# Kernel tuning notes

Hardware: AMD Instinct MI355X
Metric: run time of the kernel (lower is better)

The kernel has to match this reference:

```python
import jax, jax.numpy as jnp
import numpy as np
import math

B, S, D, H = 2, 2048, 1024, 16
HD = D // H
WINDOW_LEFT = 256   # window_size=(256,-1): only left constraint active
NEG = -1e9


def rotate_half(x):
    x1, x2 = jnp.split(x, 2, axis=-1)
    return jnp.concatenate([-x2, x1], axis=-1)


def setup_inputs() -> dict:
    key = jax.random.key(0)
    ks = jax.random.split(key, 10)
    x = jax.random.normal(ks[0], (B, S, D), dtype=jnp.float32)
    mask = jnp.ones((B, S), dtype=bool)
    cos = jax.random.uniform(ks[1], (B, S, HD), dtype=jnp.float32)
    sin = jax.random.uniform(ks[2], (B, S, HD), dtype=jnp.float32)
    sc = 1.0 / math.sqrt(D)
    Wq = jax.random.normal(ks[3], (D, D), dtype=jnp.float32) * sc
    bq = jax.random.normal(ks[4], (D,), dtype=jnp.float32) * 0.02
    Wk = jax.random.normal(ks[5], (D, D), dtype=jnp.float32) * sc
    Wv = jax.random.normal(ks[6], (D, D), dtype=jnp.float32) * sc
    bv = jax.random.normal(ks[7], (D,), dtype=jnp.float32) * 0.02
    Wo = jax.random.normal(ks[8], (D, D), dtype=jnp.float32) * sc
    bo = jax.random.normal(ks[9], (D,), dtype=jnp.float32) * 0.02
    return {"x": x, "mask": mask, "cos": cos, "sin": sin,
            "Wq": Wq, "bq": bq, "Wk": Wk, "Wv": Wv, "bv": bv,
            "Wo": Wo, "bo": bo}


def reference(x, mask, cos, sin, Wq, bq, Wk, Wv, bv, Wo, bo):
    batch, seq_len, embed_dim = x.shape
    scale = 1.0 / math.sqrt(HD)

    q = x @ Wq + bq          # [b,s,d], bias on q
    k = x @ Wk               # no bias on k
    v = x @ Wv + bv          # bias on v

    def split_heads(t):
        return jnp.swapaxes(t.reshape(batch, seq_len, H, HD), 1, 2)  # [b,h,s,hd]

    q, k, v = split_heads(q), split_heads(k), split_heads(v)

    c = cos[:, None, :, :]   # [b,1,s,hd]
    s_ = sin[:, None, :, :]
    q = q * c + rotate_half(q) * s_
    k = k * c + rotate_half(k) * s_

    scores = jnp.einsum('bhqd,bhkd->bhqk', q, k) * scale
    # padding mask over keys
    scores = jnp.where(mask[:, None, None, :], scores, NEG)
    # causal + sliding-window (left=256) masks combined
    pos = jnp.arange(seq_len)
    rel = pos[None, :] - pos[:, None]          # k - q
    keep = (rel <= 0) & (rel >= -WINDOW_LEFT)  # causal AND window-left
    scores = jnp.where(keep, scores, NEG)

    weights = jax.nn.softmax(scores, axis=-1)
    context = jnp.einsum('bhqk,bhkd->bhqd', weights, v)
    context = jnp.swapaxes(context, 1, 2).reshape(batch, seq_len, embed_dim)
    out = context @ Wo + bo
    out = out * mask[..., None]
    return out
```

## Files before the change

kernel.cpp:

```cpp
#include <hip/hip_runtime.h>
#include <cstdint>
#include <cstddef>

typedef __bf16 bf16;
typedef bf16 bf16x4 __attribute__((ext_vector_type(4)));
typedef bf16 bf16x8 __attribute__((ext_vector_type(8)));
typedef float f32x4 __attribute__((ext_vector_type(4)));

#define S_LEN 2048
#define DIM   1024
#define NHEAD 16
#define HDIM  64

__device__ __forceinline__ f32x4 mfma16(bf16x8 a, bf16x8 b, f32x4 c) {
    return __builtin_amdgcn_mfma_f32_16x16x32_bf16(a, b, c, 0, 0, 0);
}

__device__ __forceinline__ float exp2fast(float x) {
    return __builtin_amdgcn_exp2f(x);
}

__device__ __forceinline__ void gload_lds16(const bf16* g, bf16* l) {
    __builtin_amdgcn_global_load_lds(
        (const __attribute__((address_space(1))) unsigned*)g,
        (__attribute__((address_space(3))) unsigned*)l, 16, 0, 0);
}

__global__ __launch_bounds__(256) void cvt_x_kernel(const float* __restrict__ x,
                                                    bf16* __restrict__ xb) {
    int i = blockIdx.x * 256 + threadIdx.x;
    float4 v = ((const float4*)x)[i];
    bf16x4 o = { (bf16)v.x, (bf16)v.y, (bf16)v.z, (bf16)v.w };
    ((bf16x4*)xb)[i] = o;
}

__global__ __launch_bounds__(256) void wt_kernel(const float* __restrict__ Wq, const float* __restrict__ Wk,
                                                 const float* __restrict__ Wv, const float* __restrict__ Wo,
                                                 bf16* __restrict__ WqT, bf16* __restrict__ WkT,
                                                 bf16* __restrict__ WvT, bf16* __restrict__ WoT) {
    const float* W; bf16* WT;
    int z = blockIdx.z;
    if      (z == 0) { W = Wq; WT = WqT; }
    else if (z == 1) { W = Wk; WT = WkT; }
    else if (z == 2) { W = Wv; WT = WvT; }
    else             { W = Wo; WT = WoT; }
    __shared__ bf16 tile[64][72];
    int k0 = blockIdx.x * 64, n0 = blockIdx.y * 64;
    int t = threadIdx.x;
#pragma unroll
    for (int p = 0; p < 4; ++p) {
        int task = p * 256 + t;
        int ki = task >> 4, nj = (task & 15) * 4;
        float4 v = *(const float4*)(W + (size_t)(k0 + ki) * DIM + n0 + nj);
        tile[ki][nj + 0] = (bf16)v.x; tile[ki][nj + 1] = (bf16)v.y;
        tile[ki][nj + 2] = (bf16)v.z; tile[ki][nj + 3] = (bf16)v.w;
    }
    __syncthreads();
#pragma unroll
    for (int p = 0; p < 4; ++p) {
        int task = p * 256 + t;
        int ni = task >> 4, kj = (task & 15) * 4;
        bf16x4 o = { tile[kj + 0][ni], tile[kj + 1][ni], tile[kj + 2][ni], tile[kj + 3][ni] };
        *(bf16x4*)(WT + (size_t)(n0 + ni) * DIM + k0 + kj) = o;
    }
}

__device__ __forceinline__ void stage256(const bf16* __restrict__ A, const bf16* __restrict__ BT,
                                         int m0, int n0, int k0, int t, int w, bf16* dst) {
#pragma unroll
    for (int i = 0; i < 4; ++i) {
        int c = i * 512 + t;
        int row = c >> 3;
        int colb = ((c & 7) * 16) ^ ((row & 7) << 4);
        gload_lds16(A + (size_t)(m0 + row) * DIM + k0 + (colb >> 1), dst + i * 4096 + w * 512);
    }
#pragma unroll
    for (int i = 0; i < 4; ++i) {
        int c = i * 512 + t;
        int row = c >> 3;
        int colb = ((c & 7) * 16) ^ ((row & 7) << 4);
        gload_lds16(BT + (size_t)(n0 + row) * DIM + k0 + (colb >> 1), dst + 16384 + i * 4096 + w * 512);
    }
}

__global__ __launch_bounds__(512, 2) void gemm_qkv_kernel(const bf16* __restrict__ xb,
                                                          const bf16* __restrict__ WallT,
                                                          const float* __restrict__ bq, const float* __restrict__ bv,
                                                          const float* __restrict__ cosp, const float* __restrict__ sinp,
                                                          bf16* __restrict__ qT, bf16* __restrict__ kT,
                                                          bf16* __restrict__ vT) {
    __shared__ bf16 lds[2][32768];
    int t = threadIdx.x, lane = t & 63, w = t >> 6;
    int wr = w >> 2, wc = w & 3;
    int lc = lane & 15, lr = lane >> 4;
    int bid = blockIdx.x;
    int swz = (bid & 7) * 24 + (bid >> 3);
    int bx = swz / 12, by = swz % 12;
    int m0 = bx * 256, n0 = by * 256;

    f32x4 acc[8][4] = {};
    const int aswz = (lc & 7) << 4;

    stage256(xb, WallT, m0, n0, 0, t, w, lds[0]);
    asm volatile("s_waitcnt vmcnt(0)" ::: "memory");
    __builtin_amdgcn_s_barrier();
    __builtin_amdgcn_sched_barrier(0);

    const int NT = DIM / 64;
    for (int kt = 0; kt < NT; ++kt) {
        if (kt + 1 < NT) stage256(xb, WallT, m0, n0, (kt + 1) * 64, t, w, lds[(kt + 1) & 1]);
        const char* bufb = (const char*)lds[kt & 1];
        bf16x8 aF[4], bF[4];
#pragma unroll
        for (int ks = 0; ks < 2; ++ks) {
#pragma unroll
            for (int nf = 0; nf < 4; ++nf) {
                int row = wc * 64 + nf * 16 + lc;
                bF[nf] = *(const bf16x8*)(bufb + 32768 + ((row * 128 + ks * 64 + lr * 16) ^ aswz));
            }
#pragma unroll
            for (int half = 0; half < 2; ++half) {
#pragma unroll
                for (int m4 = 0; m4 < 4; ++m4) {
                    int row = wr * 128 + (half * 4 + m4) * 16 + lc;
                    aF[m4] = *(const bf16x8*)(bufb + ((row * 128 + ks * 64 + lr * 16) ^ aswz));
                }
                __builtin_amdgcn_s_setprio(1);
#pragma unroll
                for (int m4 = 0; m4 < 4; ++m4)
#pragma unroll
                    for (int nf = 0; nf < 4; ++nf)
                        acc[half * 4 + m4][nf] = mfma16(aF[m4], bF[nf], acc[half * 4 + m4][nf]);
                __builtin_amdgcn_s_setprio(0);
            }
        }
        if (kt + 1 < NT) {
            asm volatile("s_waitcnt vmcnt(0)" ::: "memory");
            __builtin_amdgcn_s_barrier();
            __builtin_amdgcn_sched_barrier(0);
        }
    }

    int z = by >> 2;
    int h = (by & 3) * 4 + wc;
    int row0 = m0 + wr * 128 + lr * 4;
    if (z < 2) {
        bf16* qkT = (z == 0) ? qT : kT;
#pragma unroll
        for (int nf = 0; nf < 2; ++nf) {
            int hd1 = nf * 16 + lc;
            float b1 = (z == 0) ? bq[h * HDIM + hd1] : 0.0f;
            float b2 = (z == 0) ? bq[h * HDIM + hd1 + 32] : 0.0f;
#pragma unroll
            for (int mf = 0; mf < 8; ++mf) {
#pragma unroll
                for (int r = 0; r < 4; ++r) {
                    int bs = row0 + mf * 16 + r;
                    size_t cb = (size_t)bs * HDIM + hd1;
                    float c1 = cosp[cb], s1 = sinp[cb];
                    float c2 = cosp[cb + 32], s2 = sinp[cb + 32];
                    float v1 = acc[mf][nf][r] + b1;
                    float v2 = acc[mf][nf + 2][r] + b2;
                    int b = bs >> 11, s = bs & (S_LEN - 1);
                    size_t o = ((size_t)(b * NHEAD + h) * S_LEN + s) * HDIM;
                    qkT[o + hd1]      = (bf16)(v1 * c1 - v2 * s1);
                    qkT[o + hd1 + 32] = (bf16)(v2 * c2 + v1 * s2);
                }
            }
        }
    } else {
#pragma unroll
        for (int nf = 0; nf < 4; ++nf) {
            int hd = nf * 16 + lc;
            float bvv = bv[h * HDIM + hd];
#pragma unroll
            for (int mf = 0; mf < 8; ++mf) {
                bf16x4 o;
#pragma unroll
                for (int r = 0; r < 4; ++r) o[r] = (bf16)(acc[mf][nf][r] + bvv);
                int bs = row0 + mf * 16;
                int b = bs >> 11, s = bs & (S_LEN - 1);
                *(bf16x4*)(vT + ((size_t)((b * NHEAD + h) * HDIM + hd)) * S_LEN + s) = o;
            }
        }
    }
}

__device__ __forceinline__ void stage_tile(const bf16* __restrict__ A, const bf16* __restrict__ BT,
                                           int m0, int n0, int k0,
                                           bf16* sA, bf16* sB, int w, int lane) {
#pragma unroll
    for (int p = 0; p < 2; ++p) {
        int c = p * 256 + w * 64 + lane;
        const bf16* ga = A + (size_t)(m0 + (c >> 2)) * DIM + k0 + (c & 3) * 8;
        gload_lds16(ga, sA + (p * 256 + w * 64) * 8);
        const bf16* gb = BT + (size_t)(n0 + (c >> 2)) * DIM + k0 + (c & 3) * 8;
        gload_lds16(gb, sB + (p * 256 + w * 64) * 8);
    }
}

__device__ __forceinline__ void gemm_main(const bf16* __restrict__ A, const bf16* __restrict__ BT,
                                          int m0, int n0, f32x4 acc[4][4]) {
    __shared__ bf16 sA[3][128 * 32];
    __shared__ bf16 sB[3][128 * 32];
    int t = threadIdx.x;
    int lane = t & 63, w = t >> 6;
    int wr = w >> 1, wc = w & 1;
    int lc = lane & 15, lr = lane >> 4;
    const int NSTEP = DIM / 32;

    stage_tile(A, BT, m0, n0, 0,  sA[0], sB[0], w, lane);
    stage_tile(A, BT, m0, n0, 32, sA[1], sB[1], w, lane);

    int rs = 0, ss = 2;
    for (int kt = 0; kt < NSTEP; ++kt) {
        if (kt < NSTEP - 1) asm volatile("s_waitcnt vmcnt(4)" ::: "memory");
        else                asm volatile("s_waitcnt vmcnt(0)" ::: "memory");
        __builtin_amdgcn_s_barrier();
        asm volatile("" ::: "memory");
        if (kt < NSTEP - 2)
            stage_tile(A, BT, m0, n0, (kt + 2) * 32, sA[ss], sB[ss], w, lane);

        const bf16* pa = sA[rs] + (wr * 64 + lc) * 32 + lr * 8;
        const bf16* pb = sB[rs] + (wc * 64 + lc) * 32 + lr * 8;
        bf16x8 af[4], bfr[4];
#pragma unroll
        for (int m = 0; m < 4; ++m) af[m] = *(const bf16x8*)(pa + m * 16 * 32);
#pragma unroll
        for (int n = 0; n < 4; ++n) bfr[n] = *(const bf16x8*)(pb + n * 16 * 32);
#pragma unroll
        for (int m = 0; m < 4; ++m)
#pragma unroll
            for (int n = 0; n < 4; ++n)
                acc[m][n] = mfma16(af[m], bfr[n], acc[m][n]);
        rs = (rs == 2) ? 0 : rs + 1;
        ss = (ss == 2) ? 0 : ss + 1;
    }
}

__global__ __launch_bounds__(256, 3) void gemm_out_kernel(const bf16* __restrict__ ctx, const bf16* __restrict__ WoT,
                                                          const float* __restrict__ bo, float* __restrict__ out) {
    int m0 = blockIdx.x * 128, n0 = blockIdx.y * 128;
    f32x4 acc[4][4] = {};
    gemm_main(ctx, WoT, m0, n0, acc);
    int t = threadIdx.x;
    int lane = t & 63, w = t >> 6;
    int wr = w >> 1, wc = w & 1;
    int lc = lane & 15, lr = lane >> 4;
    int row0 = m0 + wr * 64 + lr * 4;
    int col0 = n0 + wc * 64 + lc;
#pragma unroll
    for (int nf = 0; nf < 4; ++nf) {
        int col = col0 + nf * 16;
        float bvv = bo[col];
#pragma unroll
        for (int mf = 0; mf < 4; ++mf)
#pragma unroll
            for (int r = 0; r < 4; ++r)
                out[(size_t)(row0 + mf * 16 + r) * DIM + col] = acc[mf][nf][r] + bvv;
    }
}

__global__ __launch_bounds__(64) void attn_kernel(const bf16* __restrict__ qT, const bf16* __restrict__ kT,
                                                  const bf16* __restrict__ vT, bf16* __restrict__ ctx) {
    int q0 = blockIdx.x * 32;
    int bh = blockIdx.y;
    int b = bh >> 4, h = bh & 15;
    int lane = threadIdx.x;
    int lc = lane & 15, lr = lane >> 4;
    __shared__ bf16 sP[32 * 64];
    char* sPb = (char*)sP;
    const bf16* Qb = qT + (size_t)bh * S_LEN * HDIM;
    const bf16* Kb = kT + (size_t)bh * S_LEN * HDIM;
    const bf16* Vb = vT + (size_t)bh * HDIM * S_LEN;

    const float SCL = 0.125f * 1.44269504089f;
    const int swz = (lc & 7) << 4;

    bf16x8 qf[2][2];
#pragma unroll
    for (int mf = 0; mf < 2; ++mf)
#pragma unroll
        for (int kk = 0; kk < 2; ++kk)
            qf[mf][kk] = *(const bf16x8*)(Qb + (size_t)(q0 + mf * 16 + lc) * HDIM + kk * 32 + lr * 8);

    f32x4 accO[2][4] = {};
    float mrun[2] = { -30000.0f, -30000.0f };
    float lrun[2] = { 0.0f, 0.0f };

    int klo = (q0 >= 256) ? ((q0 - 256) >> 6) : 0;
    int khi = (q0 + 31) >> 6;

    bf16x8 kfc[8], kfn[8], vf[8];
#pragma unroll
    for (int nf = 0; nf < 4; ++nf)
#pragma unroll
        for (int kk = 0; kk < 2; ++kk)
            kfc[nf * 2 + kk] = *(const bf16x8*)(Kb + (size_t)(klo * 64 + nf * 16 + lc) * HDIM + kk * 32 + lr * 8);

    for (int kt = klo; kt <= khi; ++kt) {
        int kbase = kt * 64;
#pragma unroll
        for (int n4 = 0; n4 < 4; ++n4)
#pragma unroll
            for (int kk = 0; kk < 2; ++kk)
                vf[n4 * 2 + kk] = *(const bf16x8*)(Vb + (size_t)(n4 * 16 + lc) * S_LEN + kbase + kk * 32 + lr * 8);
        if (kt < khi) {
#pragma unroll
            for (int nf = 0; nf < 4; ++nf)
#pragma unroll
                for (int kk = 0; kk < 2; ++kk)
                    kfn[nf * 2 + kk] = *(const bf16x8*)(Kb + (size_t)(kbase + 64 + nf * 16 + lc) * HDIM + kk * 32 + lr * 8);
        }

        f32x4 sacc[2][4] = {};
        __builtin_amdgcn_s_setprio(1);
#pragma unroll
        for (int nf = 0; nf < 4; ++nf)
#pragma unroll
            for (int kk = 0; kk < 2; ++kk) {
                sacc[0][nf] = mfma16(kfc[nf * 2 + kk], qf[0][kk], sacc[0][nf]);
                sacc[1][nf] = mfma16(kfc[nf * 2 + kk], qf[1][kk], sacc[1][nf]);
            }
        __builtin_amdgcn_s_setprio(0);
#pragma unroll
        for (int mf = 0; mf < 2; ++mf) {
            int qi = q0 + mf * 16 + lc;
#pragma unroll
            for (int nf = 0; nf < 4; ++nf)
#pragma unroll
                for (int r = 0; r < 4; ++r) {
                    int ki = kbase + nf * 16 + lr * 4 + r;
                    bool keep = (ki <= qi) && (ki >= qi - 256);
                    sacc[mf][nf][r] = keep ? sacc[mf][nf][r] * SCL : -30000.0f;
                }
        }
#pragma unroll
        for (int mf = 0; mf < 2; ++mf) {
            float mx = sacc[mf][0][0];
#pragma unroll
            for (int nf = 0; nf < 4; ++nf)
#pragma unroll
                for (int r = 0; r < 4; ++r) mx = fmaxf(mx, sacc[mf][nf][r]);
            mx = fmaxf(mx, __shfl_xor(mx, 16));
            mx = fmaxf(mx, __shfl_xor(mx, 32));
            float mnew = fmaxf(mrun[mf], mx);
            float alpha = exp2fast(mrun[mf] - mnew);
            mrun[mf] = mnew;
            float rsum = 0.0f;
#pragma unroll
            for (int nf = 0; nf < 4; ++nf)
#pragma unroll
                for (int r = 0; r < 4; ++r) {
                    float e = exp2fast(sacc[mf][nf][r] - mnew);
                    sacc[mf][nf][r] = e;
                    rsum += e;
                }
            rsum += __shfl_xor(rsum, 16);
            rsum += __shfl_xor(rsum, 32);
            lrun[mf] = lrun[mf] * alpha + rsum;
            float aq[4];
#pragma unroll
            for (int r = 0; r < 4; ++r) aq[r] = __shfl(alpha, lr * 4 + r);
#pragma unroll
            for (int n4 = 0; n4 < 4; ++n4)
#pragma unroll
                for (int r = 0; r < 4; ++r) accO[mf][n4][r] *= aq[r];
        }
#pragma unroll
        for (int mf = 0; mf < 2; ++mf)
#pragma unroll
            for (int nf = 0; nf < 4; ++nf) {
                bf16x4 o = { (bf16)sacc[mf][nf][0], (bf16)sacc[mf][nf][1],
                             (bf16)sacc[mf][nf][2], (bf16)sacc[mf][nf][3] };
                int wb = ((mf * 16 + lc) * 64 + nf * 16 + lr * 4) * 2;
                *(bf16x4*)(sPb + (wb ^ swz)) = o;
            }
        asm volatile("s_waitcnt lgkmcnt(0)" ::: "memory");
        bf16x8 pf[2][2];
#pragma unroll
        for (int mf = 0; mf < 2; ++mf)
#pragma unroll
            for (int kk = 0; kk < 2; ++kk) {
                int rb = ((mf * 16 + lc) * 64 + kk * 32 + lr * 8) * 2;
                pf[mf][kk] = *(const bf16x8*)(sPb + (rb ^ swz));
            }
        __builtin_amdgcn_s_setprio(1);
#pragma unroll
        for (int n4 = 0; n4 < 4; ++n4)
#pragma unroll
            for (int kk = 0; kk < 2; ++kk) {
                accO[0][n4] = mfma16(pf[0][kk], vf[n4 * 2 + kk], accO[0][n4]);
                accO[1][n4] = mfma16(pf[1][kk], vf[n4 * 2 + kk], accO[1][n4]);
            }
        __builtin_amdgcn_s_setprio(0);
#pragma unroll
        for (int i = 0; i < 8; ++i) kfc[i] = kfn[i];
    }
#pragma unroll
    for (int mf = 0; mf < 2; ++mf) {
        float linv = 1.0f / lrun[mf];
        float lq[4];
#pragma unroll
        for (int r = 0; r < 4; ++r) lq[r] = __shfl(linv, lr * 4 + r);
#pragma unroll
        for (int n4 = 0; n4 < 4; ++n4)
#pragma unroll
            for (int r = 0; r < 4; ++r) {
                int s = q0 + mf * 16 + lr * 4 + r;
                int d = n4 * 16 + lc;
                ctx[((size_t)(b * S_LEN + s)) * DIM + h * HDIM + d] = (bf16)(accO[mf][n4][r] * lq[r]);
            }
    }
}

extern "C" void kernel_launch(void* const* d_in, const int* in_sizes, int n_in,
                              void* d_out, int out_size, void* d_ws, size_t ws_size,
                              hipStream_t stream) {
    const float* x    = (const float*)d_in[0];
    const float* cosp = (const float*)d_in[2];
    const float* sinp = (const float*)d_in[3];
    const float* Wq   = (const float*)d_in[4];
    const float* bq   = (const float*)d_in[5];
    const float* Wk   = (const float*)d_in[6];
    const float* Wv   = (const float*)d_in[7];
    const float* bv   = (const float*)d_in[8];
    const float* Wo   = (const float*)d_in[9];
    const float* bo   = (const float*)d_in[10];
    float* out = (float*)d_out;

    char* ws = (char*)d_ws;
    const size_t MB = 1ull << 20;
    bf16* xb  = (bf16*)(ws + 0 * MB);
    bf16* WqT = (bf16*)(ws + 8 * MB);
    bf16* WkT = (bf16*)(ws + 10 * MB);
    bf16* WvT = (bf16*)(ws + 12 * MB);
    bf16* WoT = (bf16*)(ws + 14 * MB);
    bf16* qT  = (bf16*)(ws + 16 * MB);
    bf16* kT  = (bf16*)(ws + 24 * MB);
    bf16* vT  = (bf16*)(ws + 32 * MB);
    bf16* ctx = (bf16*)(ws + 40 * MB);

    cvt_x_kernel<<<4096, 256, 0, stream>>>(x, xb);
    wt_kernel<<<dim3(16, 16, 4), 256, 0, stream>>>(Wq, Wk, Wv, Wo, WqT, WkT, WvT, WoT);
    gemm_qkv_kernel<<<192, 512, 0, stream>>>(xb, WqT, bq, bv, cosp, sinp, qT, kT, vT);
    attn_kernel<<<dim3(64, 32), 64, 0, stream>>>(qT, kT, vT, ctx);
    gemm_out_kernel<<<dim3(32, 8), 256, 0, stream>>>(ctx, WoT, bo, out);
}
```

Measured before the change: 103.9 us.

## Split QKV GEMM K-stages into half-units with finer-grained pipelined loads and XCD-aware attention mapping

Restructures the QKV GEMM main loop so each 64-wide K step is loaded as two 32-wide units. The second unit is issued after the first is consumed, with vmcnt-based partial waits instead of a full drain each step. It also changes the LDS swizzle to a 64-element row layout, removes the L2-oriented block swizzle in the QKV GEMM, and remaps attention blocks so heads are grouped per XCD. The weight pointer is renamed from WallT to Wall, which may imply a layout change on the host side not shown here. The extra barriers per step add sync overhead in exchange for better overlap of loads and MFMA work.

```diff
diff --git a/kernel.cpp b/kernel.cpp
--- a/kernel.cpp
+++ b/kernel.cpp
@@ -65,26 +65,8 @@
     }
 }
 
-__device__ __forceinline__ void stage256(const bf16* __restrict__ A, const bf16* __restrict__ BT,
-                                         int m0, int n0, int k0, int t, int w, bf16* dst) {
-#pragma unroll
-    for (int i = 0; i < 4; ++i) {
-        int c = i * 512 + t;
-        int row = c >> 3;
-        int colb = ((c & 7) * 16) ^ ((row & 7) << 4);
-        gload_lds16(A + (size_t)(m0 + row) * DIM + k0 + (colb >> 1), dst + i * 4096 + w * 512);
-    }
-#pragma unroll
-    for (int i = 0; i < 4; ++i) {
-        int c = i * 512 + t;
-        int row = c >> 3;
-        int colb = ((c & 7) * 16) ^ ((row & 7) << 4);
-        gload_lds16(BT + (size_t)(n0 + row) * DIM + k0 + (colb >> 1), dst + 16384 + i * 4096 + w * 512);
-    }
-}
-
 __global__ __launch_bounds__(512, 2) void gemm_qkv_kernel(const bf16* __restrict__ xb,
-                                                          const bf16* __restrict__ WallT,
+                                                          const bf16* __restrict__ Wall,
                                                           const float* __restrict__ bq, const float* __restrict__ bv,
                                                           const float* __restrict__ cosp, const float* __restrict__ sinp,
                                                           bf16* __restrict__ qT, bf16* __restrict__ kT,
@@ -94,52 +76,96 @@
     int wr = w >> 2, wc = w & 3;
     int lc = lane & 15, lr = lane >> 4;
     int bid = blockIdx.x;
-    int swz = (bid & 7) * 24 + (bid >> 3);
-    int bx = swz / 12, by = swz % 12;
+    int bx = bid / 12, by = bid % 12;
     int m0 = bx * 256, n0 = by * 256;
 
+    int i0 = t, i1 = 512 + t;
+    int r0 = i0 >> 2, r1 = i1 >> 2;
+    int ke0 = (((i0 & 3) ^ (r0 & 3)) << 3);
+    int ke1 = (((i1 & 3) ^ (r1 & 3)) << 3);
+    const bf16* srcA0 = xb   + (size_t)(m0 + r0) * DIM + ke0;
+    const bf16* srcA1 = xb   + (size_t)(m0 + r1) * DIM + ke1;
+    const bf16* srcB0 = Wall + (size_t)(n0 + r0) * DIM + ke0;
+    const bf16* srcB1 = Wall + (size_t)(n0 + r1) * DIM + ke1;
+
+#define STAGE_UNIT(kt_, u_) {                                              \
+        bf16* d = (bf16*)lds[(kt_) & 1] + (u_) * 8192 + w * 512;           \
+        int ko = (kt_) * 64 + (u_) * 32;                                   \
+        gload_lds16(srcA0 + ko, d);                                        \
+        gload_lds16(srcB0 + ko, d + 16384);                                \
+        gload_lds16(srcA1 + ko, d + 4096);                                 \
+        gload_lds16(srcB1 + ko, d + 4096 + 16384);                         \
+    }
+
     f32x4 acc[8][4] = {};
-    const int aswz = (lc & 7) << 4;
-
-    stage256(xb, WallT, m0, n0, 0, t, w, lds[0]);
-    asm volatile("s_waitcnt vmcnt(0)" ::: "memory");
-    __builtin_amdgcn_s_barrier();
-    __builtin_amdgcn_sched_barrier(0);
+    const int aoff = (lr * 16) ^ ((lc & 3) << 4);
+    const int arow = (wr * 128 + lc) * 64;
+    const int brow = 32768 + (wc * 64 + lc) * 64;
 
     const int NT = DIM / 64;
+    STAGE_UNIT(0, 0);
+    STAGE_UNIT(0, 1);
+
     for (int kt = 0; kt < NT; ++kt) {
-        if (kt + 1 < NT) stage256(xb, WallT, m0, n0, (kt + 1) * 64, t, w, lds[(kt + 1) & 1]);
-        const char* bufb = (const char*)lds[kt & 1];
+        asm volatile("s_waitcnt vmcnt(4)" ::: "memory");
+        __builtin_amdgcn_s_barrier();
+        asm volatile("" ::: "memory");
+        if (kt + 1 < NT) STAGE_UNIT(kt + 1, 0);
+        const char* base = (const char*)lds[kt & 1];
         bf16x8 aF[4], bF[4];
 #pragma unroll
-        for (int ks = 0; ks < 2; ++ks) {
-#pragma unroll
-            for (int nf = 0; nf < 4; ++nf) {
-                int row = wc * 64 + nf * 16 + lc;
-                bF[nf] = *(const bf16x8*)(bufb + 32768 + ((row * 128 + ks * 64 + lr * 16) ^ aswz));
-            }
-#pragma unroll
-            for (int half = 0; half < 2; ++half) {
-#pragma unroll
-                for (int m4 = 0; m4 < 4; ++m4) {
-                    int row = wr * 128 + (half * 4 + m4) * 16 + lc;
-                    aF[m4] = *(const bf16x8*)(bufb + ((row * 128 + ks * 64 + lr * 16) ^ aswz));
-                }
-                __builtin_amdgcn_s_setprio(1);
-#pragma unroll
-                for (int m4 = 0; m4 < 4; ++m4)
-#pragma unroll
-                    for (int nf = 0; nf < 4; ++nf)
-                        acc[half * 4 + m4][nf] = mfma16(aF[m4], bF[nf], acc[half * 4 + m4][nf]);
-                __builtin_amdgcn_s_setprio(0);
-            }
-        }
-        if (kt + 1 < NT) {
-            asm volatile("s_waitcnt vmcnt(0)" ::: "memory");
-            __builtin_amdgcn_s_barrier();
-            __builtin_amdgcn_sched_barrier(0);
-        }
-    }
+        for (int nf = 0; nf < 4; ++nf)
+            bF[nf] = *(const bf16x8*)(base + brow + nf * 1024 + aoff);
+#pragma unroll
+        for (int m4 = 0; m4 < 4; ++m4)
+            aF[m4] = *(const bf16x8*)(base + arow + m4 * 1024 + aoff);
+        __builtin_amdgcn_s_setprio(1);
+#pragma unroll
+        for (int m4 = 0; m4 < 4; ++m4)
+#pragma unroll
+            for (int nf = 0; nf < 4; ++nf)
+                acc[m4][nf] = mfma16(aF[m4], bF[nf], acc[m4][nf]);
+        __builtin_amdgcn_s_setprio(0);
+#pragma unroll
+        for (int m4 = 0; m4 < 4; ++m4)
+            aF[m4] = *(const bf16x8*)(base + arow + 4096 + m4 * 1024 + aoff);
+        __builtin_amdgcn_s_setprio(1);
+#pragma unroll
+        for (int m4 = 0; m4 < 4; ++m4)
+#pragma unroll
+            for (int nf = 0; nf < 4; ++nf)
+                acc[4 + m4][nf] = mfma16(aF[m4], bF[nf], acc[4 + m4][nf]);
+        __builtin_amdgcn_s_setprio(0);
+        if (kt + 1 < NT) asm volatile("s_waitcnt vmcnt(4)" ::: "memory");
+        else             asm volatile("s_waitcnt vmcnt(0)" ::: "memory");
+        __builtin_amdgcn_s_barrier();
+        asm volatile("" ::: "memory");
+        if (kt + 1 < NT) STAGE_UNIT(kt + 1, 1);
+#pragma unroll
+        for (int nf = 0; nf < 4; ++nf)
+            bF[nf] = *(const bf16x8*)(base + 16384 + brow + nf * 1024 + aoff);
+#pragma unroll
+        for (int m4 = 0; m4 < 4; ++m4)
+            aF[m4] = *(const bf16x8*)(base + 16384 + arow + m4 * 1024 + aoff);
+        __builtin_amdgcn_s_setprio(1);
+#pragma unroll
+        for (int m4 = 0; m4 < 4; ++m4)
+#pragma unroll
+            for (int nf = 0; nf < 4; ++nf)
+                acc[m4][nf] = mfma16(aF[m4], bF[nf], acc[m4][nf]);
+        __builtin_amdgcn_s_setprio(0);
+#pragma unroll
+        for (int m4 = 0; m4 < 4; ++m4)
+            aF[m4] = *(const bf16x8*)(base + 16384 + arow + 4096 + m4 * 1024 + aoff);
+        __builtin_amdgcn_s_setprio(1);
+#pragma unroll
+        for (int m4 = 0; m4 < 4; ++m4)
+#pragma unroll
+            for (int nf = 0; nf < 4; ++nf)
+                acc[4 + m4][nf] = mfma16(aF[m4], bF[nf], acc[4 + m4][nf]);
+        __builtin_amdgcn_s_setprio(0);
+    }
+#undef STAGE_UNIT
 
     int z = by >> 2;
     int h = (by & 3) * 4 + wc;
@@ -199,18 +225,20 @@
     }
 }
 
-__device__ __forceinline__ void gemm_main(const bf16* __restrict__ A, const bf16* __restrict__ BT,
-                                          int m0, int n0, f32x4 acc[4][4]) {
+__global__ __launch_bounds__(256, 3) void gemm_out_kernel(const bf16* __restrict__ ctx, const bf16* __restrict__ WoT,
+                                                          const float* __restrict__ bo, float* __restrict__ out) {
     __shared__ bf16 sA[3][128 * 32];
     __shared__ bf16 sB[3][128 * 32];
+    int m0 = blockIdx.x * 128, n0 = blockIdx.y * 128;
     int t = threadIdx.x;
     int lane = t & 63, w = t >> 6;
     int wr = w >> 1, wc = w & 1;
     int lc = lane & 15, lr = lane >> 4;
     const int NSTEP = DIM / 32;
 
-    stage_tile(A, BT, m0, n0, 0,  sA[0], sB[0], w, lane);
-    stage_tile(A, BT, m0, n0, 32, sA[1], sB[1], w, lane);
+    f32x4 acc[4][4] = {};
+    stage_tile(ctx, WoT, m0, n0, 0,  sA[0], sB[0], w, lane);
+    stage_tile(ctx, WoT, m0, n0, 32, sA[1], sB[1], w, lane);
 
     int rs = 0, ss = 2;
     for (int kt = 0; kt < NSTEP; ++kt) {
@@ -219,7 +247,7 @@
         __builtin_amdgcn_s_barrier();
         asm volatile("" ::: "memory");
         if (kt < NSTEP - 2)
-            stage_tile(A, BT, m0, n0, (kt + 2) * 32, sA[ss], sB[ss], w, lane);
+            stage_tile(ctx, WoT, m0, n0, (kt + 2) * 32, sA[ss], sB[ss], w, lane);
 
         const bf16* pa = sA[rs] + (wr * 64 + lc) * 32 + lr * 8;
         const bf16* pb = sB[rs] + (wc * 64 + lc) * 32 + lr * 8;
@@ -236,17 +264,7 @@
         rs = (rs == 2) ? 0 : rs + 1;
         ss = (ss == 2) ? 0 : ss + 1;
     }
-}
-
-__global__ __launch_bounds__(256, 3) void gemm_out_kernel(const bf16* __restrict__ ctx, const bf16* __restrict__ WoT,
-                                                          const float* __restrict__ bo, float* __restrict__ out) {
-    int m0 = blockIdx.x * 128, n0 = blockIdx.y * 128;
-    f32x4 acc[4][4] = {};
-    gemm_main(ctx, WoT, m0, n0, acc);
-    int t = threadIdx.x;
-    int lane = t & 63, w = t >> 6;
-    int wr = w >> 1, wc = w & 1;
-    int lc = lane & 15, lr = lane >> 4;
+
     int row0 = m0 + wr * 64 + lr * 4;
     int col0 = n0 + wc * 64 + lc;
 #pragma unroll
@@ -263,8 +281,10 @@
 
 __global__ __launch_bounds__(64) void attn_kernel(const bf16* __restrict__ qT, const bf16* __restrict__ kT,
                                                   const bf16* __restrict__ vT, bf16* __restrict__ ctx) {
-    int q0 = blockIdx.x * 32;
-    int bh = blockIdx.y;
+    int bid = blockIdx.x + 64 * blockIdx.y;
+    int xcd = bid & 7, idx = bid >> 3;
+    int bh = xcd * 4 + (idx >> 6);
+    int q0 = (idx & 63) * 32;
     int b = bh >> 4, h = bh & 15;
     int lane = threadIdx.x;
     int lc = lane & 15, lr = lane >> 4;
```

After: 100.9 us. 1.03x faster.
